# Performance work log

Measured on AMD Instinct MI355X. Metric: run time of the kernel, lower is better.

## Reference

```python
import jax, jax.numpy as jnp
import numpy as np

N_NODES = 50000


def setup_inputs() -> dict:
    key = jax.random.key(0)
    k1, k2, k3 = jax.random.split(key, 3)
    x = jax.random.normal(k1, (N_NODES, 128), dtype=jnp.float32)
    edge_index = jax.random.randint(k2, (2, 800000), 0, N_NODES, dtype=jnp.int64)
    weight = jax.random.normal(k3, (128, 128), dtype=jnp.float32) * (1.0 / np.sqrt(128))
    bias = jnp.zeros((128,), dtype=jnp.float32)
    return {"x": x, "edge_index": edge_index, "weight": weight, "bias": bias}


def reference(x, edge_index, weight, bias):
    # GCNConv (PyG defaults): add self-loops, sym-normalize, linear, scatter-add, bias; then ReLU.
    N = x.shape[0]
    self_loops = jnp.arange(N, dtype=edge_index.dtype)
    row = jnp.concatenate([edge_index[0], self_loops])  # source nodes [E+N]
    col = jnp.concatenate([edge_index[1], self_loops])  # target nodes [E+N]

    # degree over targets (edge weights are all ones), includes self-loops -> deg >= 1
    deg = jax.ops.segment_sum(jnp.ones_like(col, dtype=x.dtype), col, num_segments=N)
    dinv = jax.lax.rsqrt(deg)
    norm = dinv[row] * dinv[col]  # [E+N]

    h = x @ weight  # [N, nhid] linear transform before propagation
    msgs = h[row] * norm[:, None]  # gather + scale, [E+N, nhid]
    out = jax.ops.segment_sum(msgs, col, num_segments=N) + bias  # scatter-add aggregate
    return jax.nn.relu(out)
```

## Files before the change

kernel.cpp:

```cpp
#include <hip/hip_runtime.h>

#define NFEAT 128
#define CAP 64

typedef __attribute__((ext_vector_type(8))) short short8;
typedef __attribute__((ext_vector_type(4))) float f32x4;
typedef __attribute__((ext_vector_type(4))) float f32x4v;
typedef __attribute__((ext_vector_type(2))) float f32x2v;

__device__ inline short f2bf(float f) {
    unsigned u = __builtin_bit_cast(unsigned, f);
    u += 0x7FFFu + ((u >> 16) & 1u);
    return (short)(u >> 16);
}
__device__ inline float bf2f(unsigned short u) {
    return __builtin_bit_cast(float, ((unsigned)u) << 16);
}

__global__ void prep_kernel(const float* __restrict__ W, unsigned short* __restrict__ Wt,
                            unsigned int* __restrict__ cnt, int N) {
    int i = blockIdx.x * 256 + threadIdx.x;
    if (i < N) cnt[i] = 0u;
    if (i < NFEAT * NFEAT) {
        int k = i >> 7, n = i & 127;
        Wt[n * NFEAT + k] = (unsigned short)f2bf(W[k * NFEAT + n]);
    }
}

__global__ void __launch_bounds__(256)
gemm_countfill_kernel(const float* __restrict__ x,
                      const unsigned short* __restrict__ Wt,
                      unsigned short* __restrict__ h, int N, int gb,
                      const int* __restrict__ row, const int* __restrict__ col,
                      int E, unsigned int* __restrict__ cnt,
                      unsigned short* __restrict__ bucket) {
    __shared__ unsigned short tile[4][16][136];
    int bid = blockIdx.x;

    if (bid >= gb) {
        int e0 = (bid - gb) * 512 + threadIdx.x;
        int e1 = e0 + 256;
        int c0 = 0, c1 = 0;
        bool v0 = e0 < E, v1 = e1 < E;
        if (v0) c0 = col[e0];
        if (v1) c1 = col[e1];
        unsigned int t0 = 0, t1 = 0;
        if (v0) t0 = atomicAdd(&cnt[c0], 1u);
        if (v1) t1 = atomicAdd(&cnt[c1], 1u);
        if (v0 && t0 < CAP) bucket[(size_t)c0 * CAP + t0] = (unsigned short)row[e0];
        if (v1 && t1 < CAP) bucket[(size_t)c1 * CAP + t1] = (unsigned short)row[e1];
        return;
    }

    int wave = threadIdx.x >> 6;
    int lane = threadIdx.x & 63;
    int li = lane & 15;
    int kg = lane >> 4;
    int m0 = bid * 64 + wave * 16;
    int arow = m0 + li;
    int srow = (arow < N) ? arow : (N - 1);

    f32x4 acc[8];
    #pragma unroll
    for (int nt = 0; nt < 8; ++nt) acc[nt] = (f32x4){0.f, 0.f, 0.f, 0.f};

    #pragma unroll
    for (int ks = 0; ks < 4; ++ks) {
        const f32x4v* xp = (const f32x4v*)(x + (size_t)srow * NFEAT + ks * 32 + kg * 8);
        f32x4v f0 = __builtin_nontemporal_load(xp);
        f32x4v f1 = __builtin_nontemporal_load(xp + 1);
        short8 a;
        a[0] = f2bf(f0.x); a[1] = f2bf(f0.y); a[2] = f2bf(f0.z); a[3] = f2bf(f0.w);
        a[4] = f2bf(f1.x); a[5] = f2bf(f1.y); a[6] = f2bf(f1.z); a[7] = f2bf(f1.w);
        #pragma unroll
        for (int nt = 0; nt < 8; ++nt) {
            short8 b = *(const short8*)(Wt + (size_t)(nt * 16 + li) * NFEAT + ks * 32 + kg * 8);
            acc[nt] = __builtin_amdgcn_mfma_f32_16x16x32_bf16(a, b, acc[nt], 0, 0, 0);
        }
    }

    #pragma unroll
    for (int r = 0; r < 4; ++r) {
        #pragma unroll
        for (int nt = 0; nt < 8; ++nt)
            tile[wave][kg * 4 + r][nt * 16 + li] = (unsigned short)f2bf(acc[nt][r]);
    }
    __syncthreads();

    int rr = lane >> 2;
    int orow = m0 + rr;
    #pragma unroll
    for (int cc = 0; cc < 4; ++cc) {
        int chunk = cc * 4 + (lane & 3);
        if (orow < N) {
            short8 v = *(const short8*)&tile[wave][rr][chunk * 8];
            *(short8*)(h + (size_t)orow * NFEAT + chunk * 8) = v;
        }
    }
}

__global__ void aggregate_kernel(const unsigned short* __restrict__ h,
                                 const unsigned short* __restrict__ bucket,
                                 const unsigned int* __restrict__ cnt,
                                 const float* __restrict__ bias,
                                 float* __restrict__ out, int N) {
    int wid = threadIdx.x >> 6;
    int lane = threadIdx.x & 63;
    int c = blockIdx.x * 4 + wid;
    if (c >= N) return;
    int grp = lane >> 4;
    int li = lane & 15;
    int col0 = li * 8;
    int n = (int)cnt[c];
    float dc = rsqrtf((float)(n + 1));
    if (n > CAP) n = CAP;
    const unsigned short* bk = bucket + (size_t)c * CAP;

    float acc[8];
    if (grp == 0) {
        short8 v = *(const short8*)(h + (size_t)c * NFEAT + col0);
        #pragma unroll
        for (int i = 0; i < 8; ++i) acc[i] = bf2f((unsigned short)v[i]) * dc;
    } else {
        #pragma unroll
        for (int i = 0; i < 8; ++i) acc[i] = 0.f;
    }

    for (int j = 0; j < n; j += 16) {
        int idx[4];
        bool p[4];
        float dr[4];
        short8 v[4];
        #pragma unroll
        for (int k = 0; k < 4; ++k) {
            int jj = j + grp + k * 4;
            p[k] = jj < n;
            idx[k] = p[k] ? (int)bk[jj] : 0;
        }
        #pragma unroll
        for (int k = 0; k < 4; ++k) {
            if (p[k]) {
                v[k] = *(const short8*)(h + (size_t)idx[k] * NFEAT + col0);
                dr[k] = rsqrtf((float)(cnt[idx[k]] + 1u));
            }
        }
        #pragma unroll
        for (int k = 0; k < 4; ++k) {
            if (p[k]) {
                #pragma unroll
                for (int i = 0; i < 8; ++i) acc[i] += bf2f((unsigned short)v[k][i]) * dr[k];
            }
        }
    }

    #pragma unroll
    for (int i = 0; i < 8; ++i) {
        acc[i] += __shfl_xor(acc[i], 16, 64);
        acc[i] += __shfl_xor(acc[i], 32, 64);
    }

    float a0, a1;
    switch (grp) {
        case 0: a0 = acc[0]; a1 = acc[1]; break;
        case 1: a0 = acc[2]; a1 = acc[3]; break;
        case 2: a0 = acc[4]; a1 = acc[5]; break;
        default: a0 = acc[6]; a1 = acc[7]; break;
    }
    const float2* bp = (const float2*)(bias + col0 + grp * 2);
    float2 b = *bp;
    f32x2v o;
    o.x = fmaxf(a0 * dc + b.x, 0.f);
    o.y = fmaxf(a1 * dc + b.y, 0.f);
    __builtin_nontemporal_store(o, (f32x2v*)(out + (size_t)c * NFEAT + col0 + grp * 2));
}

extern "C" void kernel_launch(void* const* d_in, const int* in_sizes, int n_in,
                              void* d_out, int out_size, void* d_ws, size_t ws_size,
                              hipStream_t stream) {
    const float* x    = (const float*)d_in[0];
    const int*   ei   = (const int*)d_in[1];
    const float* W    = (const float*)d_in[2];
    const float* bias = (const float*)d_in[3];
    float* out = (float*)d_out;

    int N = in_sizes[0] / NFEAT;
    int E = in_sizes[1] / 2;
    const int* row = ei;
    const int* col = ei + E;

    char* ws = (char*)d_ws;
    size_t o = 0;
    unsigned int*   cnt    = (unsigned int*)(ws + o);   o += (size_t)N * 4;
    unsigned short* Wt     = (unsigned short*)(ws + o); o += (size_t)NFEAT * NFEAT * 2;
    unsigned short* bucket = (unsigned short*)(ws + o); o += (size_t)N * CAP * 2;
    unsigned short* h      = (unsigned short*)(ws + o);

    int nb = (N + 255) / 256;
    int gb = (N + 63) / 64;
    int cb = (E + 511) / 512;

    prep_kernel<<<nb, 256, 0, stream>>>(W, Wt, cnt, N);
    gemm_countfill_kernel<<<gb + cb, 256, 0, stream>>>(x, Wt, h, N, gb,
                                                       row, col, E, cnt, bucket);
    aggregate_kernel<<<(N + 3) / 4, 256, 0, stream>>>(h, bucket, cnt, bias, out, N);
}
```

Baseline: 108.0 us.

## Partition bucket fill and aggregation by XCD-local node ranges

The count/fill stage becomes XCD-aware. Each of 1024 blocks gets a role from its block index mod 8 and scans an edge chunk, keeping only edges whose target lies in that role's node range, so atomics and bucket writes for a node range stay on one XCD's L2. Aggregation blocks are mapped so that each XCD handles the same contiguous node range. In exchange, every edge's col is read 8 times across roles, and the correctness of the L2-locality intent rests on blocks being assigned to XCDs round-robin.

Result: slower. 125.2 us (+16.0%).

```diff
diff --git a/kernel.cpp b/kernel.cpp
--- a/kernel.cpp
+++ b/kernel.cpp
@@ -2,6 +2,7 @@
 
 #define NFEAT 128
 #define CAP 64
+#define NXCD 8
 
 typedef __attribute__((ext_vector_type(8))) short short8;
 typedef __attribute__((ext_vector_type(4))) float f32x4;
@@ -30,7 +31,7 @@
 __global__ void __launch_bounds__(256)
 gemm_countfill_kernel(const float* __restrict__ x,
                       const unsigned short* __restrict__ Wt,
-                      unsigned short* __restrict__ h, int N, int gb,
+                      unsigned short* __restrict__ h, int N, int gb, int cb,
                       const int* __restrict__ row, const int* __restrict__ col,
                       int E, unsigned int* __restrict__ cnt,
                       unsigned short* __restrict__ bucket) {
@@ -38,17 +39,23 @@
     int bid = blockIdx.x;
 
     if (bid >= gb) {
-        int e0 = (bid - gb) * 512 + threadIdx.x;
-        int e1 = e0 + 256;
-        int c0 = 0, c1 = 0;
-        bool v0 = e0 < E, v1 = e1 < E;
-        if (v0) c0 = col[e0];
-        if (v1) c1 = col[e1];
-        unsigned int t0 = 0, t1 = 0;
-        if (v0) t0 = atomicAdd(&cnt[c0], 1u);
-        if (v1) t1 = atomicAdd(&cnt[c1], 1u);
-        if (v0 && t0 < CAP) bucket[(size_t)c0 * CAP + t0] = (unsigned short)row[e0];
-        if (v1 && t1 < CAP) bucket[(size_t)c1 * CAP + t1] = (unsigned short)row[e1];
+        int k = bid - gb;
+        int role = bid & (NXCD - 1);
+        int q = k >> 3;
+        int G = cb >> 3;
+        int rlo = (int)((long long)N * role / NXCD);
+        int rhi = (int)((long long)N * (role + 1) / NXCD);
+        int chunk = (E + G - 1) / G;
+        int e0 = q * chunk;
+        int e1 = min(e0 + chunk, E);
+        for (int e = e0 + (int)threadIdx.x; e < e1; e += 256) {
+            int c = __builtin_nontemporal_load(col + e);
+            if (c >= rlo && c < rhi) {
+                int r = __builtin_nontemporal_load(row + e);
+                unsigned int t = atomicAdd(&cnt[c], 1u);
+                if (t < CAP) bucket[(size_t)c * CAP + t] = (unsigned short)r;
+            }
+        }
         return;
     }
 
@@ -106,8 +113,12 @@
                                  float* __restrict__ out, int N) {
     int wid = threadIdx.x >> 6;
     int lane = threadIdx.x & 63;
-    int c = blockIdx.x * 4 + wid;
-    if (c >= N) return;
+    int role = blockIdx.x & (NXCD - 1);
+    int j = blockIdx.x >> 3;
+    int rlo = (int)((long long)N * role / NXCD);
+    int rhi = (int)((long long)N * (role + 1) / NXCD);
+    int c = rlo + j * 4 + wid;
+    if (c >= rhi) return;
     int grp = lane >> 4;
     int li = lane & 15;
     int col0 = li * 8;
@@ -126,14 +137,14 @@
         for (int i = 0; i < 8; ++i) acc[i] = 0.f;
     }
 
-    for (int j = 0; j < n; j += 16) {
+    for (int j2 = 0; j2 < n; j2 += 16) {
         int idx[4];
         bool p[4];
         float dr[4];
         short8 v[4];
         #pragma unroll
         for (int k = 0; k < 4; ++k) {
-            int jj = j + grp + k * 4;
+            int jj = j2 + grp + k * 4;
             p[k] = jj < n;
             idx[k] = p[k] ? (int)bk[jj] : 0;
         }
@@ -197,10 +208,13 @@
 
     int nb = (N + 255) / 256;
     int gb = (N + 63) / 64;
-    int cb = (E + 511) / 512;
+    int cb = 1024;
 
     prep_kernel<<<nb, 256, 0, stream>>>(W, Wt, cnt, N);
-    gemm_countfill_kernel<<<gb + cb, 256, 0, stream>>>(x, Wt, h, N, gb,
+    gemm_countfill_kernel<<<gb + cb, 256, 0, stream>>>(x, Wt, h, N, gb, cb,
                                                        row, col, E, cnt, bucket);
-    aggregate_kernel<<<(N + 3) / 4, 256, 0, stream>>>(h, bucket, cnt, bias, out, N);
-}
+
+    int maxRange = (N + NXCD - 1) / NXCD;
+    int ab = NXCD * ((maxRange + 3) / 4);
+    aggregate_kernel<<<ab, 256, 0, stream>>>(h, bucket, cnt, bias, out, N);
+}
```
